# Kernel optimization log

Measured on AMD Instinct MI355X. Metric: run time of the kernel, lower is better.

The kernel has to match this reference:

```python
import jax, jax.numpy as jnp
import numpy as np

INPUT_SIZE = 4
HIDDEN_SIZE = 64
OUTPUT_SIZE = 40
BATCH = 4096
SEQ_LEN = 512


def setup_inputs() -> dict:
    key = jax.random.key(0)
    ks = jax.random.split(key, 7)
    s_ih = 1.0 / np.sqrt(HIDDEN_SIZE)
    x = jax.random.normal(ks[0], (BATCH, SEQ_LEN, INPUT_SIZE), dtype=jnp.float32)
    # PyTorch nn.RNN params, uniform(-1/sqrt(H), 1/sqrt(H))
    W_ih = jax.random.uniform(ks[1], (HIDDEN_SIZE, INPUT_SIZE), minval=-s_ih, maxval=s_ih, dtype=jnp.float32)
    W_hh = jax.random.uniform(ks[2], (HIDDEN_SIZE, HIDDEN_SIZE), minval=-s_ih, maxval=s_ih, dtype=jnp.float32)
    b_ih = jax.random.uniform(ks[3], (HIDDEN_SIZE,), minval=-s_ih, maxval=s_ih, dtype=jnp.float32)
    b_hh = jax.random.uniform(ks[4], (HIDDEN_SIZE,), minval=-s_ih, maxval=s_ih, dtype=jnp.float32)
    fc_W = jax.random.uniform(ks[5], (OUTPUT_SIZE, HIDDEN_SIZE), minval=-s_ih, maxval=s_ih, dtype=jnp.float32)
    fc_b = jax.random.uniform(ks[6], (OUTPUT_SIZE,), minval=-s_ih, maxval=s_ih, dtype=jnp.float32)
    return {"x": x, "W_ih": W_ih, "W_hh": W_hh, "b_ih": b_ih, "b_hh": b_hh, "fc_W": fc_W, "fc_b": fc_b}


def reference(x, W_ih, W_hh, b_ih, b_hh, fc_W, fc_b):
    B = x.shape[0]
    # Precompute input projections for all timesteps: [T, B, H]
    xp = jnp.einsum('bti,hi->tbh', x, W_ih) + (b_ih + b_hh)

    def step(h, xp_t):
        h = jnp.tanh(xp_t + h @ W_hh.T)
        return h, None

    h0 = jnp.zeros((B, HIDDEN_SIZE), dtype=x.dtype)
    h_last, _ = jax.lax.scan(step, h0, xp)
    # fc on last timestep hidden state
    return h_last @ fc_W.T + fc_b
```

## Files before the change

### kernel.cpp

```cpp
#include <hip/hip_runtime.h>
#include <math.h>

#define BATCH 4096
#define SEQ_T 512
#define ISZ   4
#define HID   64
#define OSZ   40
#define RPB   16

typedef __attribute__((ext_vector_type(8))) _Float16     half8;
typedef __attribute__((ext_vector_type(2))) _Float16     half2v;
typedef __attribute__((ext_vector_type(4))) float        float4v;
typedef __attribute__((ext_vector_type(2))) unsigned int uint2v;

static __device__ __forceinline__ half2v pk_f16(float a, float b) {
    return __builtin_bit_cast(half2v, __builtin_amdgcn_cvt_pkrtz(a, b));
}

static __device__ __forceinline__ float fast_tanh_s(float s) {
    float e = __builtin_amdgcn_exp2f(s);
    return fmaf(-2.0f, __builtin_amdgcn_rcpf(e + 1.0f), 1.0f);
}

#define LDS_BARRIER() asm volatile("s_waitcnt lgkmcnt(0)\n\ts_barrier" ::: "memory")

__global__ __launch_bounds__(512, 1)
void rnn_f16x2_kernel(const float* __restrict__ x,
                      const float* __restrict__ W_ih,
                      const float* __restrict__ W_hh,
                      const float* __restrict__ b_ih,
                      const float* __restrict__ b_hh,
                      const float* __restrict__ fc_W,
                      const float* __restrict__ fc_b,
                      float* __restrict__ out)
{
    __shared__ __attribute__((aligned(16))) _Float16 hterm[2][8][16][8];
    __shared__ __attribute__((aligned(16))) float hf[16][68];

    const int tid  = threadIdx.x;
    const int grp  = tid >> 8;
    const int wg   = (tid >> 6) & 3;
    const int lane = tid & 63;
    const int n    = lane & 15;
    const int q    = lane >> 4;
    const int blk0 = blockIdx.x * RPB;
    const float SC = 2.885390081777927f;

    {
        unsigned int* p = (unsigned int*)hterm;
        #pragma unroll
        for (int i = tid; i < (int)(sizeof(hterm) / 4); i += 512) p[i] = 0u;
    }

    half8 A10, A11, A20, A21;
    {
        const float* wr = W_hh + (16 * wg + n) * HID;
        #pragma unroll
        for (int j = 0; j < 8; ++j) {
            float f0 = SC * wr[     8 * q + j];
            float f1 = SC * wr[32 + 8 * q + j];
            _Float16 h0 = (_Float16)f0; A10[j] = h0; A20[j] = (_Float16)(f0 - (float)h0);
            _Float16 h1 = (_Float16)f1; A11[j] = h1; A21[j] = (_Float16)(f1 - (float)h1);
        }
    }

    const int r0 = 16 * wg + 4 * q;
    float wih[4][4], bias[4];
    #pragma unroll
    for (int r = 0; r < 4; ++r) {
        bias[r] = SC * (b_ih[r0 + r] + b_hh[r0 + r]);
        #pragma unroll
        for (int i = 0; i < ISZ; ++i) wih[r][i] = SC * W_ih[(r0 + r) * ISZ + i];
    }

    const float* xrow = x + (size_t)(blk0 + n) * SEQ_T * ISZ;
    float4v xa = *(const float4v*)(xrow + (size_t)(grp    ) * ISZ);
    float4v xb = *(const float4v*)(xrow + (size_t)(grp + 2) * ISZ);
    float4v xc = *(const float4v*)(xrow + (size_t)(grp + 4) * ISZ);
    float4v xd = *(const float4v*)(xrow + (size_t)(grp + 6) * ISZ);
    int tnext = grp + 8;

    const int gw = 2 * wg + (q >> 1);
    const int j0 = 4 * (q & 1);

    float p0, p1, p2, p3;
    float hl0 = 0.f, hl1 = 0.f, hl2 = 0.f, hl3 = 0.f;

    __syncthreads();

#define MFMA16(A, B, C) __builtin_amdgcn_mfma_f32_16x16x32_f16((A), (B), (C), 0, 0, 0)

#define XP_FROM(XR)                                                            \
    {                                                                          \
        p0 = bias[0]; p1 = bias[1]; p2 = bias[2]; p3 = bias[3];                \
        _Pragma("unroll")                                                      \
        for (int i = 0; i < ISZ; ++i) {                                        \
            p0 = fmaf(XR[i], wih[0][i], p0);                                   \
            p1 = fmaf(XR[i], wih[1][i], p1);                                   \
            p2 = fmaf(XR[i], wih[2][i], p2);                                   \
            p3 = fmaf(XR[i], wih[3][i], p3);                                   \
        }                                                                      \
    }

#define XRELOAD(XR)                                                            \
    {                                                                          \
        int tn = tnext; if (tn > SEQ_T - 1) tn = SEQ_T - 1;                    \
        XR = *(const float4v*)(xrow + (size_t)tn * ISZ);                       \
        tnext += 2;                                                            \
    }

#define ACTIVE_STEP(RB, WB)                                                    \
    {                                                                          \
        __builtin_amdgcn_s_setprio(1);                                         \
        half8 B10 = *(const half8*)&hterm[RB][    q][n][0];                    \
        half8 B11 = *(const half8*)&hterm[RB][4 + q][n][0];                    \
        const float4v zz = {0.f, 0.f, 0.f, 0.f};                               \
        float4v cx = {p0, p1, p2, p3};                                         \
        float4v aA = MFMA16(A10, B10, cx);                                     \
        float4v aB = MFMA16(A11, B11, zz);                                     \
        float4v aC = MFMA16(A20, B10, zz);                                     \
        float4v aD = MFMA16(A21, B11, zz);                                     \
        float4v sj = (aA + aB) + (aC + aD);                                    \
        hl0 = fast_tanh_s(sj[0]); hl1 = fast_tanh_s(sj[1]);                    \
        hl2 = fast_tanh_s(sj[2]); hl3 = fast_tanh_s(sj[3]);                    \
        half2v hi01 = pk_f16(hl0, hl1), hi23 = pk_f16(hl2, hl3);               \
        uint2v whi = { __builtin_bit_cast(unsigned int, hi01),                 \
                       __builtin_bit_cast(unsigned int, hi23) };               \
        *(uint2v*)&hterm[WB][gw][n][j0] = whi;                                 \
        __builtin_amdgcn_s_setprio(0);                                         \
    }

    if (grp == 0) {
        XP_FROM(xa); XRELOAD(xa);
        for (int it = 0; it < SEQ_T / 2; it += 4) {
            ACTIVE_STEP(0, 1); LDS_BARRIER(); XP_FROM(xb); XRELOAD(xb); LDS_BARRIER();
            ACTIVE_STEP(0, 1); LDS_BARRIER(); XP_FROM(xc); XRELOAD(xc); LDS_BARRIER();
            ACTIVE_STEP(0, 1); LDS_BARRIER(); XP_FROM(xd); XRELOAD(xd); LDS_BARRIER();
            ACTIVE_STEP(0, 1); LDS_BARRIER(); XP_FROM(xa); XRELOAD(xa); LDS_BARRIER();
        }
    } else {
        for (int it = 0; it < SEQ_T / 2; it += 4) {
            XP_FROM(xa); XRELOAD(xa); LDS_BARRIER(); ACTIVE_STEP(1, 0); LDS_BARRIER();
            XP_FROM(xb); XRELOAD(xb); LDS_BARRIER(); ACTIVE_STEP(1, 0); LDS_BARRIER();
            XP_FROM(xc); XRELOAD(xc); LDS_BARRIER(); ACTIVE_STEP(1, 0); LDS_BARRIER();
            XP_FROM(xd); XRELOAD(xd); LDS_BARRIER(); ACTIVE_STEP(1, 0); LDS_BARRIER();
        }
    }
#undef ACTIVE_STEP
#undef XRELOAD
#undef XP_FROM
#undef MFMA16

    if (grp == 1) {
        float4v hv = {hl0, hl1, hl2, hl3};
        *(float4v*)&hf[n][r0] = hv;
    }
    __syncthreads();
    for (int it = tid; it < RPB * OSZ; it += 512) {
        const int b = it / OSZ;
        const int o = it - b * OSZ;
        const float* wo = fc_W + o * HID;
        float acc = fc_b[o];
        #pragma unroll
        for (int j = 0; j < HID; ++j)
            acc = fmaf(hf[b][j], wo[j], acc);
        out[(size_t)(blk0 + b) * OSZ + o] = acc;
    }
}

extern "C" void kernel_launch(void* const* d_in, const int* in_sizes, int n_in,
                              void* d_out, int out_size, void* d_ws, size_t ws_size,
                              hipStream_t stream) {
    const float* x    = (const float*)d_in[0];
    const float* W_ih = (const float*)d_in[1];
    const float* W_hh = (const float*)d_in[2];
    const float* b_ih = (const float*)d_in[3];
    const float* b_hh = (const float*)d_in[4];
    const float* fc_W = (const float*)d_in[5];
    const float* fc_b = (const float*)d_in[6];
    float* out = (float*)d_out;

    rnn_f16x2_kernel<<<BATCH / RPB, 512, 0, stream>>>(
        x, W_ih, W_hh, b_ih, b_hh, fc_W, fc_b, out);
}
```

Before: 192.1 us.

## Replace block-wide barriers with per-wave LDS flag polling between ping-pong groups

Replaces the two s_barrier calls per timestep with monotonically increasing per-wave flags in LDS. Each wave polls until all four producer waves have published the expected step counter, then runs its step and publishes its own flag. The intent is to drop full-workgroup barrier overhead and let the two groups synchronise only on their real data dependency. The cost is spin-polling on LDS and a dependence on LDS write ordering for correctness. There is also a hazard: a single flag slot per wave is shared by both the reader and writer phases, so a fast wave could overwrite a buffer before a slower wave has read it.

Result: slower. 284.4 us (+48.0%).

```diff
diff --git a/kernel.cpp b/kernel.cpp
--- a/kernel.cpp
+++ b/kernel.cpp
@@ -21,8 +21,6 @@
     float e = __builtin_amdgcn_exp2f(s);
     return fmaf(-2.0f, __builtin_amdgcn_rcpf(e + 1.0f), 1.0f);
 }
-
-#define LDS_BARRIER() asm volatile("s_waitcnt lgkmcnt(0)\n\ts_barrier" ::: "memory")
 
 __global__ __launch_bounds__(512, 1)
 void rnn_f16x2_kernel(const float* __restrict__ x,
@@ -35,6 +33,7 @@
                       float* __restrict__ out)
 {
     __shared__ __attribute__((aligned(16))) _Float16 hterm[2][8][16][8];
+    __shared__ __attribute__((aligned(16))) unsigned int hflag[4];
     __shared__ __attribute__((aligned(16))) float hf[16][68];
 
     const int tid  = threadIdx.x;
@@ -50,6 +49,7 @@
         unsigned int* p = (unsigned int*)hterm;
         #pragma unroll
         for (int i = tid; i < (int)(sizeof(hterm) / 4); i += 512) p[i] = 0u;
+        if (tid < 4) hflag[tid] = 0u;
     }
 
     half8 A10, A11, A20, A21;
@@ -89,6 +89,26 @@
     __syncthreads();
 
 #define MFMA16(A, B, C) __builtin_amdgcn_mfma_f32_16x16x32_f16((A), (B), (C), 0, 0, 0)
+
+#define POLL(UEXP)                                                             \
+    {                                                                          \
+        const unsigned int ue = (unsigned int)(UEXP);                          \
+        for (;;) {                                                             \
+            unsigned int f0 = ((volatile unsigned int*)hflag)[0];              \
+            unsigned int f1 = ((volatile unsigned int*)hflag)[1];              \
+            unsigned int f2 = ((volatile unsigned int*)hflag)[2];              \
+            unsigned int f3 = ((volatile unsigned int*)hflag)[3];              \
+            if (f0 >= ue && f1 >= ue && f2 >= ue && f3 >= ue) break;           \
+        }                                                                      \
+        asm volatile("" ::: "memory");                                         \
+    }
+
+#define FLAG_SET(UVAL)                                                         \
+    {                                                                          \
+        asm volatile("s_waitcnt lgkmcnt(0)" ::: "memory");                     \
+        if (lane == 0)                                                         \
+            ((volatile unsigned int*)hflag)[wg] = (unsigned int)(UVAL);        \
+    }
 
 #define XP_FROM(XR)                                                            \
     {                                                                          \
@@ -130,25 +150,38 @@
         __builtin_amdgcn_s_setprio(0);                                         \
     }
 
+#define STEPU(RB, WB, XR)                                                      \
+    {                                                                          \
+        POLL(ucur);                                                            \
+        ACTIVE_STEP(RB, WB);                                                   \
+        FLAG_SET(ucur + 1);                                                    \
+        ucur += 2;                                                             \
+        XP_FROM(XR); XRELOAD(XR);                                              \
+    }
+
+    int ucur = grp;
+    XP_FROM(xa); XRELOAD(xa);
     if (grp == 0) {
-        XP_FROM(xa); XRELOAD(xa);
         for (int it = 0; it < SEQ_T / 2; it += 4) {
-            ACTIVE_STEP(0, 1); LDS_BARRIER(); XP_FROM(xb); XRELOAD(xb); LDS_BARRIER();
-            ACTIVE_STEP(0, 1); LDS_BARRIER(); XP_FROM(xc); XRELOAD(xc); LDS_BARRIER();
-            ACTIVE_STEP(0, 1); LDS_BARRIER(); XP_FROM(xd); XRELOAD(xd); LDS_BARRIER();
-            ACTIVE_STEP(0, 1); LDS_BARRIER(); XP_FROM(xa); XRELOAD(xa); LDS_BARRIER();
+            STEPU(0, 1, xb)
+            STEPU(0, 1, xc)
+            STEPU(0, 1, xd)
+            STEPU(0, 1, xa)
         }
     } else {
         for (int it = 0; it < SEQ_T / 2; it += 4) {
-            XP_FROM(xa); XRELOAD(xa); LDS_BARRIER(); ACTIVE_STEP(1, 0); LDS_BARRIER();
-            XP_FROM(xb); XRELOAD(xb); LDS_BARRIER(); ACTIVE_STEP(1, 0); LDS_BARRIER();
-            XP_FROM(xc); XRELOAD(xc); LDS_BARRIER(); ACTIVE_STEP(1, 0); LDS_BARRIER();
-            XP_FROM(xd); XRELOAD(xd); LDS_BARRIER(); ACTIVE_STEP(1, 0); LDS_BARRIER();
+            STEPU(1, 0, xb)
+            STEPU(1, 0, xc)
+            STEPU(1, 0, xd)
+            STEPU(1, 0, xa)
         }
     }
+#undef STEPU
 #undef ACTIVE_STEP
 #undef XRELOAD
 #undef XP_FROM
+#undef FLAG_SET
+#undef POLL
 #undef MFMA16
 
     if (grp == 1) {
```
